# Kernel optimization log

Hardware: AMD Instinct MI355X
Metric: run time of the kernel (lower is better)

The kernel has to match this reference:

```python
import jax, jax.numpy as jnp
import numpy as np

B, S, D, H, F = 2, 2048, 1024, 16, 4096
DK = D // H
EPS = 1e-6


def _ln(x, g, b):
    mu = jnp.mean(x, axis=-1, keepdims=True)
    var = jnp.mean(jnp.square(x - mu), axis=-1, keepdims=True)
    return (x - mu) * jax.lax.rsqrt(var + EPS) * g + b


def setup_inputs() -> dict:
    key = jax.random.key(0)
    ks = jax.random.split(key, 8)
    sc = 0.02
    return {
        "x": jax.random.normal(ks[0], (B, S, D), jnp.float32),
        "wq": jax.random.normal(ks[1], (D, D), jnp.float32) * sc,
        "bq": jnp.zeros((D,), jnp.float32),
        "wk": jax.random.normal(ks[2], (D, D), jnp.float32) * sc,
        "bk": jnp.zeros((D,), jnp.float32),
        "wv": jax.random.normal(ks[3], (D, D), jnp.float32) * sc,
        "bv": jnp.zeros((D,), jnp.float32),
        "wo": jax.random.normal(ks[4], (D, D), jnp.float32) * sc,
        "bo": jnp.zeros((D,), jnp.float32),
        "w1": jax.random.normal(ks[5], (D, F), jnp.float32) * sc,
        "b1": jnp.zeros((F,), jnp.float32),
        "w2": jax.random.normal(ks[6], (F, D), jnp.float32) * sc,
        "b2": jnp.zeros((D,), jnp.float32),
        "g1": jnp.ones((D,), jnp.float32),
        "be1": jnp.zeros((D,), jnp.float32),
        "g2": jnp.ones((D,), jnp.float32),
        "be2": jnp.zeros((D,), jnp.float32),
    }


def reference(x, wq, bq, wk, bk, wv, bv, wo, bo, w1, b1, w2, b2, g1, be1, g2, be2):
    # Multi-head self-attention (no masks, eval-mode dropout = identity)
    q = (x @ wq + bq).reshape(B, S, H, DK)
    k = (x @ wk + bk).reshape(B, S, H, DK)
    v = (x @ wv + bv).reshape(B, S, H, DK)
    scale = 1.0 / (DK ** 0.5)
    score = jnp.einsum('bihd,bjhd->bhij', q, k) * scale  # [B,H,S,S]
    p = jax.nn.softmax(score, axis=-1)
    attn = jnp.einsum('bhij,bjhd->bihd', p, v).reshape(B, S, D)
    attn = attn @ wo + bo
    # residual + LayerNorm 1
    h = _ln(x + attn, g1, be1)
    # FFN (relu) + residual + LayerNorm 2
    ff = jax.nn.relu(h @ w1 + b1) @ w2 + b2
    return _ln(h + ff, g2, be2)
```

## Files before the change

kernel.cpp:

```cpp
#include <hip/hip_runtime.h>
#include <hip/hip_bf16.h>
#include <cmath>

typedef __bf16 bf16_t;
typedef __bf16 bf16x4 __attribute__((ext_vector_type(4)));
typedef __bf16 bf16x8 __attribute__((ext_vector_type(8)));
typedef float  f32x4  __attribute__((ext_vector_type(4)));

__device__ __forceinline__ void gld_lds16(const bf16_t* g, bf16_t* l) {
    __builtin_amdgcn_global_load_lds(
        (const __attribute__((address_space(1))) void*)g,
        (__attribute__((address_space(3))) void*)l,
        16, 0, 0);
}

struct PrepArgs {
    const float* w[6]; bf16_t* wt[6];
    int K[6], N[6], start[6];
    const float* x; bf16_t* xb; int castStart;
    const float* bq; const float* bk; float* bqkv; int biasStart;
};

__global__ __launch_bounds__(256) void prep(PrepArgs pa) {
    __shared__ float tile[32][33];
    const int bid = blockIdx.x, t = threadIdx.x;
    if (bid < pa.castStart) {
        int mi = 0;
#pragma unroll
        for (int i = 1; i < 6; i++) if (bid >= pa.start[i]) mi = i;
        const int tt  = bid - pa.start[mi];
        const int nbx = pa.N[mi] >> 5;
        const int n0 = (tt % nbx) * 32, k0 = (tt / nbx) * 32;
        const float* in = pa.w[mi];
        bf16_t* out = pa.wt[mi];
        const int K = pa.K[mi], N = pa.N[mi];
        const int tx = t & 31, ty = t >> 5;
#pragma unroll
        for (int i = 0; i < 4; i++) {
            int kk = ty + i * 8;
            tile[kk][tx] = in[(size_t)(k0 + kk) * N + n0 + tx];
        }
        __syncthreads();
#pragma unroll
        for (int i = 0; i < 4; i++) {
            int nn = ty + i * 8;
            out[(size_t)(n0 + nn) * K + k0 + tx] = (bf16_t)tile[tx][nn];
        }
    } else if (bid < pa.biasStart) {
        int i = (bid - pa.castStart) * 256 + t;
        f32x4 v = ((const f32x4*)pa.x)[i];
        bf16x4 o;
        o[0] = (bf16_t)v[0]; o[1] = (bf16_t)v[1]; o[2] = (bf16_t)v[2]; o[3] = (bf16_t)v[3];
        ((bf16x4*)pa.xb)[i] = o;
    } else {
#pragma unroll
        for (int j = 0; j < 8; j++) {
            int idx = t * 8 + j;
            pa.bqkv[idx] = idx < 1024 ? pa.bq[idx] : pa.bk[idx - 1024];
        }
    }
}

template<int BN>
__global__ __launch_bounds__(512, 2) void gemm_bt256(
    const bf16_t* __restrict__ A, const bf16_t* __restrict__ Bt,
    const float* __restrict__ bias,
    float* __restrict__ Cf, bf16_t* __restrict__ Cb,
    int M, int N, int lda, int Kloc, int relu, int nbn,
    long bt_bstride, long c_bstride) {
    constexpr int NT = BN / 64;
    constexpr int WN = BN / 4;
    __shared__ __attribute__((aligned(16))) bf16_t As[2][2][256 * 32];
    __shared__ __attribute__((aligned(16))) bf16_t Bs[2][2][BN * 32];
    const int tid  = threadIdx.x;
    const int lane = tid & 63;
    const int wave = tid >> 6;
    const int wm = wave >> 2, wn = wave & 3;
    const int kh = blockIdx.z;

    const int span  = 8 * nbn;
    const int group = blockIdx.x / span;
    const int rem   = blockIdx.x % span;
    const int bm    = group * 8 + (rem & 7);
    const int bn    = rem >> 3;

    const bf16_t* Bt_b = Bt + (size_t)blockIdx.y * bt_bstride;
    float*  Cf_b = Cf ? Cf + (size_t)blockIdx.y * c_bstride + (size_t)kh * M * N : nullptr;
    bf16_t* Cb_b = Cb ? Cb + (size_t)blockIdx.y * c_bstride : nullptr;
    const int koff = kh * Kloc;

    const int r4 = tid >> 2;
    const int kc = (tid & 3) * 8;
    const bf16_t* Ag = A    + (size_t)(bm * 256 + r4) * lda + koff + kc;
    const bf16_t* Bg = Bt_b + (size_t)(bn * BN  + r4) * lda + koff + kc;

    f32x4 acc[8][NT] = {};
    const int mrow = lane & 15;
    const int q8   = (lane >> 4) * 8;

    auto stage = [&](int kk, int buf) {
#pragma unroll
        for (int hh = 0; hh < 2; hh++) {
#pragma unroll
            for (int i = 0; i < 2; i++)
                gld_lds16(Ag + (size_t)(i * 128) * lda + kk + hh * 32,
                          &As[buf][hh][i * 128 * 32] + tid * 8);
            if (BN == 256) {
#pragma unroll
                for (int i = 0; i < 2; i++)
                    gld_lds16(Bg + (size_t)(i * 128) * lda + kk + hh * 32,
                              &Bs[buf][hh][i * 128 * 32] + tid * 8);
            } else {
                gld_lds16(Bg + kk + hh * 32, &Bs[buf][hh][0] + tid * 8);
            }
        }
    };

    stage(0, 0);
    __syncthreads();

    const int nsteps = Kloc >> 6;
    for (int st = 0; st < nsteps; ++st) {
        const int cur = st & 1;
        if (st + 1 < nsteps) stage((st + 1) << 6, cur ^ 1);

#pragma unroll
        for (int hh = 0; hh < 2; hh++) {
            bf16x8 bfr[NT];
#pragma unroll
            for (int n = 0; n < NT; n++)
                bfr[n] = *(const bf16x8*)(&Bs[cur][hh][(wn * WN + n * 16 + mrow) * 32 + q8]);
#pragma unroll
            for (int mt = 0; mt < 8; mt++) {
                bf16x8 af = *(const bf16x8*)(&As[cur][hh][(wm * 128 + mt * 16 + mrow) * 32 + q8]);
#pragma unroll
                for (int n = 0; n < NT; n++)
                    acc[mt][n] = __builtin_amdgcn_mfma_f32_16x16x32_bf16(
                        af, bfr[n], acc[mt][n], 0, 0, 0);
            }
        }
        __syncthreads();
    }

    const int rq = (lane >> 4) * 4;
#pragma unroll
    for (int mt = 0; mt < 8; mt++) {
        int row0 = bm * 256 + wm * 128 + mt * 16 + rq;
#pragma unroll
        for (int n = 0; n < NT; n++) {
            int col = bn * BN + wn * WN + n * 16 + mrow;
            float bvc = (bias && kh == 0) ? bias[col] : 0.f;
#pragma unroll
            for (int r = 0; r < 4; r++) {
                float v = acc[mt][n][r] + bvc;
                if (relu) v = fmaxf(v, 0.f);
                size_t idx = (size_t)(row0 + r) * N + col;
                if (Cf_b) Cf_b[idx] = v;
                if (Cb_b) Cb_b[idx] = (bf16_t)v;
            }
        }
    }
}

template<int MT>
__global__ __launch_bounds__(256) void gemm_bt(
    const bf16_t* __restrict__ A, const bf16_t* __restrict__ Bt,
    const float* __restrict__ bias,
    float* __restrict__ Cf, bf16_t* __restrict__ Cb,
    int M, int N, int lda, int Kloc, int relu, int nbn, int bias_row,
    long bt_bstride, long c_bstride) {
    constexpr int TM = MT * 32;
    __shared__ __attribute__((aligned(16))) bf16_t As[2][TM * 32];
    __shared__ __attribute__((aligned(16))) bf16_t Bs[2][128 * 32];
    const int tid  = threadIdx.x;
    const int lane = tid & 63;
    const int wave = tid >> 6;
    const int wm = wave & 1, wn = wave >> 1;
    const int kh = blockIdx.z;

    const int span  = 8 * nbn;
    const int group = blockIdx.x / span;
    const int rem   = blockIdx.x % span;
    const int bm    = group * 8 + (rem & 7);
    const int bn    = rem >> 3;

    const bf16_t* Bt_b = Bt + (size_t)blockIdx.y * bt_bstride;
    float*  Cf_b = Cf ? Cf + (size_t)blockIdx.y * c_bstride + (size_t)kh * M * N : nullptr;
    bf16_t* Cb_b = Cb ? Cb + (size_t)blockIdx.y * c_bstride : nullptr;
    const int koff = kh * Kloc;

    const int r4 = tid >> 2;
    const int kc = (tid & 3) * 8;
    const bf16_t* Ag = A    + (size_t)(bm * TM  + r4) * lda + koff + kc;
    const bf16_t* Bg = Bt_b + (size_t)(bn * 128 + r4) * lda + koff + kc;

    f32x4 acc[MT][4] = {};
    const int mrow = lane & 15;
    const int q8   = (lane >> 4) * 8;

    auto stage = [&](int kk, int buf) {
#pragma unroll
        for (int i = 0; i < MT / 2; i++)
            gld_lds16(Ag + (size_t)(i * 64) * lda + kk, &As[buf][i * 64 * 32] + tid * 8);
        gld_lds16(Bg + kk,                        &Bs[buf][0] + tid * 8);
        gld_lds16(Bg + (size_t)64 * lda + kk,     &Bs[buf][64 * 32] + tid * 8);
    };

    stage(0, 0);
    __syncthreads();

    const int nt = Kloc >> 5;
    for (int t7 = 0; t7 < nt; ++t7) {
        const int cur = t7 & 1;
        if (t7 + 1 < nt) stage((t7 + 1) << 5, cur ^ 1);

        bf16x8 af[MT], bfr[4];
#pragma unroll
        for (int mt = 0; mt < MT; mt++)
            af[mt] = *(const bf16x8*)(&As[cur][(wm * (MT * 16) + mt * 16 + mrow) * 32 + q8]);
#pragma unroll
        for (int nt2 = 0; nt2 < 4; nt2++)
            bfr[nt2] = *(const bf16x8*)(&Bs[cur][(wn * 64 + nt2 * 16 + mrow) * 32 + q8]);
#pragma unroll
        for (int mt = 0; mt < MT; mt++)
#pragma unroll
            for (int nt2 = 0; nt2 < 4; nt2++)
                acc[mt][nt2] = __builtin_amdgcn_mfma_f32_16x16x32_bf16(
                    af[mt], bfr[nt2], acc[mt][nt2], 0, 0, 0);

        __syncthreads();
    }

    const int rq = (lane >> 4) * 4;
#pragma unroll
    for (int mt = 0; mt < MT; mt++) {
        int row0 = bm * TM + wm * (MT * 16) + mt * 16 + rq;
#pragma unroll
        for (int nt2 = 0; nt2 < 4; nt2++) {
            int col = bn * 128 + wn * 64 + nt2 * 16 + mrow;
            float bvc = (bias && kh == 0 && !bias_row) ? bias[col] : 0.f;
#pragma unroll
            for (int r = 0; r < 4; r++) {
                float bb = (bias && kh == 0 && bias_row) ? bias[row0 + r] : bvc;
                float v = acc[mt][nt2][r] + bb;
                if (relu) v = fmaxf(v, 0.f);
                size_t idx = (size_t)(row0 + r) * N + col;
                if (Cf_b) Cf_b[idx] = v;
                if (Cb_b) Cb_b[idx] = (bf16_t)v;
            }
        }
    }
}

__global__ __launch_bounds__(256) void flash_attn_mfma(
    const bf16_t* __restrict__ QKb,
    const bf16_t* __restrict__ Vtg,
    bf16_t* __restrict__ Outb) {
    __shared__ __attribute__((aligned(16))) bf16_t Ks[2][4096];
    __shared__ __attribute__((aligned(16))) bf16_t Vs[2][4096];
    __shared__ __attribute__((aligned(16))) bf16_t Ps[4096];
    const int t = threadIdx.x;
    const int lane = t & 63, wave = t >> 6;
    const int g = lane >> 4, cl = lane & 15;
    const int b = blockIdx.z, h = blockIdx.y, q0 = blockIdx.x * 64;
    const int RS = 2048;
    const bf16_t* Qg = QKb + (size_t)(b * 2048 + q0) * RS + h * 64;
    const bf16_t* Kg = QKb + (size_t)(b * 2048) * RS + 1024 + h * 64;
    const bf16_t* Vg = Vtg + ((size_t)b * 1024 + h * 64) * 2048;

    const int sr = t >> 2;
    const int sc = (t & 3) * 8;

    const bf16_t* Qrow = Qg + (size_t)(wave * 16 + cl) * RS;
    bf16x8 qr0 = *(const bf16x8*)(Qrow + g * 8);
    bf16x8 qr1 = *(const bf16x8*)(Qrow + 32 + g * 8);

    gld_lds16(Kg + (size_t)sr * RS + sc,        &Ks[0][0]    + t * 8);
    gld_lds16(Kg + (size_t)sr * RS + 32 + sc,   &Ks[0][2048] + t * 8);
    gld_lds16(Vg + (size_t)sr * 2048 + sc,      &Vs[0][0]    + t * 8);
    gld_lds16(Vg + (size_t)sr * 2048 + 32 + sc, &Vs[0][2048] + t * 8);
    __syncthreads();

    f32x4 Oacc[4] = {};
    f32x4 Lacc = {};
    bf16x8 ones;
#pragma unroll
    for (int j = 0; j < 8; j++) ones[j] = (bf16_t)1.0f;

    const int rowb = wave * 16 + cl;
    const int psw  = (cl & 7) << 4;
    char* PsB = (char*)Ps;
    const float C = 0.125f * 1.4426950408889634f;

    for (int kt_i = 0; kt_i < 32; ++kt_i) {
        const int cur = kt_i & 1;
        if (kt_i + 1 < 32) {
            const int nb  = cur ^ 1;
            const int ktn = (kt_i + 1) * 64;
            gld_lds16(Kg + (size_t)(ktn + sr) * RS + sc,        &Ks[nb][0]    + t * 8);
            gld_lds16(Kg + (size_t)(ktn + sr) * RS + 32 + sc,   &Ks[nb][2048] + t * 8);
            gld_lds16(Vg + (size_t)sr * 2048 + ktn + sc,        &Vs[nb][0]    + t * 8);
            gld_lds16(Vg + (size_t)sr * 2048 + ktn + 32 + sc,   &Vs[nb][2048] + t * 8);
        }

        f32x4 Sacc[4] = {};
        __builtin_amdgcn_s_setprio(1);
#pragma unroll
        for (int ks = 0; ks < 2; ++ks) {
            bf16x8 bq = ks ? qr1 : qr0;
#pragma unroll
            for (int mt = 0; mt < 4; ++mt) {
                bf16x8 ak = *(const bf16x8*)(&Ks[cur][ks * 2048 + (mt * 16 + cl) * 32 + g * 8]);
                Sacc[mt] = __builtin_amdgcn_mfma_f32_16x16x32_bf16(ak, bq, Sacc[mt], 0, 0, 0);
            }
        }
        __builtin_amdgcn_s_setprio(0);

#pragma unroll
        for (int mt = 0; mt < 4; ++mt) {
            bf16x4 p4;
#pragma unroll
            for (int r = 0; r < 4; r++)
                p4[r] = (bf16_t)__builtin_amdgcn_exp2f(Sacc[mt][r] * C);
            *(bf16x4*)(PsB + ((rowb * 128 + mt * 32 + g * 8) ^ psw)) = p4;
        }

        __builtin_amdgcn_s_setprio(1);
#pragma unroll
        for (int ks = 0; ks < 2; ++ks) {
            bf16x8 ap = *(const bf16x8*)(PsB + ((rowb * 128 + ks * 64 + g * 16) ^ psw));
            Lacc = __builtin_amdgcn_mfma_f32_16x16x32_bf16(ap, ones, Lacc, 0, 0, 0);
#pragma unroll
            for (int nt = 0; nt < 4; ++nt) {
                bf16x8 bv = *(const bf16x8*)(&Vs[cur][ks * 2048 + (nt * 16 + cl) * 32 + g * 8]);
                Oacc[nt] = __builtin_amdgcn_mfma_f32_16x16x32_bf16(ap, bv, Oacc[nt], 0, 0, 0);
            }
        }
        __builtin_amdgcn_s_setprio(0);

        __syncthreads();
    }

#pragma unroll
    for (int r = 0; r < 4; r++) {
        float inv = 1.f / Lacc[r];
        int qrow = q0 + wave * 16 + g * 4 + r;
        size_t base = (size_t)(b * 2048 + qrow) * 1024 + h * 64;
#pragma unroll
        for (int nt = 0; nt < 4; nt++)
            Outb[base + nt * 16 + cl] = (bf16_t)(Oacc[nt][r] * inv);
    }
}

__global__ __launch_bounds__(256) void resid_ln3(const float* __restrict__ a,
                                                 const float* __restrict__ p0,
                                                 const float* __restrict__ p1,
                                                 const float* __restrict__ g,
                                                 const float* __restrict__ be,
                                                 float* __restrict__ outf,
                                                 bf16_t* __restrict__ outb) {
    const int row = blockIdx.x, t = threadIdx.x;
    const size_t base = (size_t)row * 1024;
    f32x4 v = ((const f32x4*)(a + base))[t] + ((const f32x4*)(p0 + base))[t];
    if (p1) v += ((const f32x4*)(p1 + base))[t];
    float sum = v[0] + v[1] + v[2] + v[3];
    float sq  = v[0] * v[0] + v[1] * v[1] + v[2] * v[2] + v[3] * v[3];
#pragma unroll
    for (int o = 1; o < 64; o <<= 1) {
        sum += __shfl_xor(sum, o);
        sq  += __shfl_xor(sq, o);
    }
    __shared__ float red[8];
    int wave = t >> 6, lane = t & 63;
    if (lane == 0) { red[wave] = sum; red[4 + wave] = sq; }
    __syncthreads();
    sum = red[0] + red[1] + red[2] + red[3];
    sq  = red[4] + red[5] + red[6] + red[7];
    float mu  = sum * (1.f / 1024.f);
    float var = sq * (1.f / 1024.f) - mu * mu;
    float rs  = rsqrtf(var + 1e-6f);
    f32x4 g4 = ((const f32x4*)g)[t];
    f32x4 b4 = ((const f32x4*)be)[t];
    f32x4 o = (v - mu) * rs * g4 + b4;
    ((f32x4*)(outf + base))[t] = o;
    if (outb) {
        bf16x4 ob;
        ob[0] = (bf16_t)o[0]; ob[1] = (bf16_t)o[1]; ob[2] = (bf16_t)o[2]; ob[3] = (bf16_t)o[3];
        ((bf16x4*)(outb + base))[t] = ob;
    }
}

extern "C" void kernel_launch(void* const* d_in, const int* in_sizes, int n_in,
                              void* d_out, int out_size, void* d_ws, size_t ws_size,
                              hipStream_t stream) {
    (void)in_sizes; (void)n_in; (void)out_size; (void)ws_size;
    const float* x   = (const float*)d_in[0];
    const float* wq  = (const float*)d_in[1];
    const float* bq  = (const float*)d_in[2];
    const float* wk  = (const float*)d_in[3];
    const float* bk  = (const float*)d_in[4];
    const float* wv  = (const float*)d_in[5];
    const float* bv  = (const float*)d_in[6];
    const float* wo  = (const float*)d_in[7];
    const float* bo  = (const float*)d_in[8];
    const float* w1  = (const float*)d_in[9];
    const float* b1  = (const float*)d_in[10];
    const float* w2  = (const float*)d_in[11];
    const float* b2  = (const float*)d_in[12];
    const float* g1  = (const float*)d_in[13];
    const float* be1 = (const float*)d_in[14];
    const float* g2  = (const float*)d_in[15];
    const float* be2 = (const float*)d_in[16];
    float* out = (float*)d_out;

    char* ws = (char*)d_ws;
    const size_t MB = 1ull << 20;
    bf16_t* xb    = (bf16_t*)(ws + 0);
    bf16_t* WtQKV = (bf16_t*)(ws + 8 * MB);
    bf16_t* WtO   = (bf16_t*)(ws + 14 * MB);
    bf16_t* Wt1   = (bf16_t*)(ws + 16 * MB);
    bf16_t* Wt2   = (bf16_t*)(ws + 24 * MB);
    float*  bqkv  = (float*)(ws + 32 * MB);
    bf16_t* QKb   = (bf16_t*)(ws + 33 * MB);
    bf16_t* Vt    = (bf16_t*)(ws + 49 * MB);
    bf16_t* ffb   = (bf16_t*)(ws + 33 * MB);
    float*  oa    = (float*)(ws + 65 * MB);
    float*  f2    = (float*)(ws + 65 * MB);
    float*  hbuf  = (float*)(ws + 97 * MB);
    bf16_t* hb    = (bf16_t*)(ws + 113 * MB);
    bf16_t* ab    = xb;
    const int MN = 4096 * 1024;

    PrepArgs pa;
    pa.w[0] = wq; pa.w[1] = wk; pa.w[2] = wv; pa.w[3] = wo; pa.w[4] = w1; pa.w[5] = w2;
    pa.wt[0] = WtQKV; pa.wt[1] = WtQKV + 1024 * 1024; pa.wt[2] = WtQKV + 2048 * 1024;
    pa.wt[3] = WtO; pa.wt[4] = Wt1; pa.wt[5] = Wt2;
    int Ks[6] = {1024, 1024, 1024, 1024, 1024, 4096};
    int Ns[6] = {1024, 1024, 1024, 1024, 4096, 1024};
    int st[6] = {0, 1024, 2048, 3072, 4096, 8192};
    for (int i = 0; i < 6; i++) { pa.K[i] = Ks[i]; pa.N[i] = Ns[i]; pa.start[i] = st[i]; }
    pa.x = x; pa.xb = xb; pa.castStart = 12288;
    pa.bq = bq; pa.bk = bk; pa.bqkv = bqkv; pa.biasStart = 12288 + 4096;
    prep<<<12288 + 4096 + 1, 256, 0, stream>>>(pa);

    gemm_bt256<128><<<256, 512, 0, stream>>>(xb, WtQKV, bqkv, nullptr, QKb,
                                        4096, 2048, 1024, 1024, 0, 16, 0, 0);
    gemm_bt<2><<<dim3(256, 2, 1), 256, 0, stream>>>(WtQKV + 2048 * 1024, xb, bv,
                                        nullptr, Vt, 1024, 2048, 1024, 1024, 0, 16, 1,
                                        (long)2048 * 1024, (long)1024 * 2048);
    flash_attn_mfma<<<dim3(32, 16, 2), 256, 0, stream>>>(QKb, Vt, ab);
    gemm_bt256<128><<<dim3(128, 1, 2), 512, 0, stream>>>(ab, WtO, bo, oa, nullptr,
                                        4096, 1024, 1024, 512, 0, 8, 0, 0);
    resid_ln3<<<4096, 256, 0, stream>>>(x, oa, oa + MN, g1, be1, hbuf, hb);
    gemm_bt256<256><<<256, 512, 0, stream>>>(hb, Wt1, b1, nullptr, ffb,
                                         4096, 4096, 1024, 1024, 1, 16, 0, 0);
    gemm_bt256<128><<<dim3(128, 1, 2), 512, 0, stream>>>(ffb, Wt2, b2, f2, nullptr,
                                        4096, 1024, 4096, 2048, 0, 8, 0, 0);
    resid_ln3<<<4096, 256, 0, stream>>>(hbuf, f2, f2 + MN, g2, be2, out, nullptr);
}
```

Before: 397.9 us.

## Add XOR-swizzled LDS layout to GEMMs and attention, 4-stage pipelined FFN1 GEMM

Applies an XOR swizzle to the 16-byte column slot used when staging tiles into LDS, and matches it on the fragment reads. This targets LDS bank conflicts in all GEMM kernels and in the flash-attention K/V reads. Adds a new gemm_deep kernel for the FFN up-projection with a 4-buffer LDS ring, explicit vmcnt waits so three stages of loads stay in flight, and setprio around the MFMA loop. The deeper ring uses more LDS and forces one block per CU, and the hand-written waitcnt counts must match the number of issued loads exactly.

```diff
diff --git a/kernel.cpp b/kernel.cpp
--- a/kernel.cpp
+++ b/kernel.cpp
@@ -13,6 +13,7 @@
         (__attribute__((address_space(3))) void*)l,
         16, 0, 0);
 }
+
 
 struct PrepArgs {
     const float* w[6]; bf16_t* wt[6];
@@ -57,6 +58,99 @@
         for (int j = 0; j < 8; j++) {
             int idx = t * 8 + j;
             pa.bqkv[idx] = idx < 1024 ? pa.bq[idx] : pa.bk[idx - 1024];
+        }
+    }
+}
+
+__global__ __launch_bounds__(512, 1) void gemm_deep(
+    const bf16_t* __restrict__ A, const bf16_t* __restrict__ Bt,
+    const float* __restrict__ bias, bf16_t* __restrict__ Cb,
+    int N, int lda, int K, int relu, int nbn) {
+    __shared__ __attribute__((aligned(16))) bf16_t As[4][256 * 32];
+    __shared__ __attribute__((aligned(16))) bf16_t Bs[4][256 * 32];
+    const int tid  = threadIdx.x;
+    const int lane = tid & 63;
+    const int wave = tid >> 6;
+    const int wm = wave >> 2, wn = wave & 3;
+
+    const int span  = 8 * nbn;
+    const int group = blockIdx.x / span;
+    const int rem   = blockIdx.x % span;
+    const int bm    = group * 8 + (rem & 7);
+    const int bn    = rem >> 3;
+
+    const int srow   = tid >> 2;
+    const int slot_s = ((tid & 3) ^ ((tid >> 3) & 3)) * 8;
+    const bf16_t* Ag = A  + (size_t)(bm * 256 + srow) * lda + slot_s;
+    const bf16_t* Bg = Bt + (size_t)(bn * 256 + srow) * lda + slot_s;
+
+    auto stage = [&](int kk, int buf) {
+        gld_lds16(Ag + kk,                       &As[buf][0]        + tid * 8);
+        gld_lds16(Ag + (size_t)128 * lda + kk,   &As[buf][128 * 32] + tid * 8);
+        gld_lds16(Bg + kk,                       &Bs[buf][0]        + tid * 8);
+        gld_lds16(Bg + (size_t)128 * lda + kk,   &Bs[buf][128 * 32] + tid * 8);
+    };
+
+    f32x4 acc[8][4] = {};
+    const int mrow = lane & 15;
+    const int qsw  = (((lane >> 4) ^ ((mrow >> 1) & 3))) * 8;
+
+    auto compute = [&](int cur) {
+        bf16x8 bfr[4], af[8];
+#pragma unroll
+        for (int n = 0; n < 4; n++)
+            bfr[n] = *(const bf16x8*)(&Bs[cur][(wn * 64 + n * 16 + mrow) * 32 + qsw]);
+#pragma unroll
+        for (int mt = 0; mt < 8; mt++)
+            af[mt] = *(const bf16x8*)(&As[cur][(wm * 128 + mt * 16 + mrow) * 32 + qsw]);
+        __builtin_amdgcn_s_setprio(1);
+#pragma unroll
+        for (int mt = 0; mt < 8; mt++)
+#pragma unroll
+            for (int n = 0; n < 4; n++)
+                acc[mt][n] = __builtin_amdgcn_mfma_f32_16x16x32_bf16(
+                    af[mt], bfr[n], acc[mt][n], 0, 0, 0);
+        __builtin_amdgcn_s_setprio(0);
+    };
+
+    stage(0, 0); stage(32, 1); stage(64, 2);
+    const int nst = K >> 5;
+    for (int t = 0; t + 3 < nst; ++t) {
+        stage((t + 3) * 32, (t + 3) & 3);
+        asm volatile("s_waitcnt vmcnt(12)" ::: "memory");
+        __builtin_amdgcn_s_barrier();
+        compute(t & 3);
+        asm volatile("s_waitcnt lgkmcnt(0)" ::: "memory");
+        __builtin_amdgcn_s_barrier();
+    }
+    asm volatile("s_waitcnt vmcnt(8)" ::: "memory");
+    __builtin_amdgcn_s_barrier();
+    compute((nst - 3) & 3);
+    asm volatile("s_waitcnt lgkmcnt(0)" ::: "memory");
+    __builtin_amdgcn_s_barrier();
+    asm volatile("s_waitcnt vmcnt(4)" ::: "memory");
+    __builtin_amdgcn_s_barrier();
+    compute((nst - 2) & 3);
+    asm volatile("s_waitcnt lgkmcnt(0)" ::: "memory");
+    __builtin_amdgcn_s_barrier();
+    asm volatile("s_waitcnt vmcnt(0)" ::: "memory");
+    __builtin_amdgcn_s_barrier();
+    compute((nst - 1) & 3);
+
+    const int rq = (lane >> 4) * 4;
+#pragma unroll
+    for (int mt = 0; mt < 8; mt++) {
+        int row0 = bm * 256 + wm * 128 + mt * 16 + rq;
+#pragma unroll
+        for (int n = 0; n < 4; n++) {
+            int col = bn * 256 + wn * 64 + n * 16 + mrow;
+            float bvc = bias ? bias[col] : 0.f;
+#pragma unroll
+            for (int r = 0; r < 4; r++) {
+                float v = acc[mt][n][r] + bvc;
+                if (relu) v = fmaxf(v, 0.f);
+                Cb[(size_t)(row0 + r) * N + col] = (bf16_t)v;
+            }
         }
     }
 }
@@ -90,13 +184,13 @@
     const int koff = kh * Kloc;
 
     const int r4 = tid >> 2;
-    const int kc = (tid & 3) * 8;
-    const bf16_t* Ag = A    + (size_t)(bm * 256 + r4) * lda + koff + kc;
-    const bf16_t* Bg = Bt_b + (size_t)(bn * BN  + r4) * lda + koff + kc;
+    const int kcs = ((tid & 3) ^ ((tid >> 3) & 3)) * 8;
+    const bf16_t* Ag = A    + (size_t)(bm * 256 + r4) * lda + koff + kcs;
+    const bf16_t* Bg = Bt_b + (size_t)(bn * BN  + r4) * lda + koff + kcs;
 
     f32x4 acc[8][NT] = {};
     const int mrow = lane & 15;
-    const int q8   = (lane >> 4) * 8;
+    const int qsw  = (((lane >> 4) ^ ((mrow >> 1) & 3))) * 8;
 
     auto stage = [&](int kk, int buf) {
 #pragma unroll
@@ -129,10 +223,10 @@
             bf16x8 bfr[NT];
 #pragma unroll
             for (int n = 0; n < NT; n++)
-                bfr[n] = *(const bf16x8*)(&Bs[cur][hh][(wn * WN + n * 16 + mrow) * 32 + q8]);
+                bfr[n] = *(const bf16x8*)(&Bs[cur][hh][(wn * WN + n * 16 + mrow) * 32 + qsw]);
 #pragma unroll
             for (int mt = 0; mt < 8; mt++) {
-                bf16x8 af = *(const bf16x8*)(&As[cur][hh][(wm * 128 + mt * 16 + mrow) * 32 + q8]);
+                bf16x8 af = *(const bf16x8*)(&As[cur][hh][(wm * 128 + mt * 16 + mrow) * 32 + qsw]);
 #pragma unroll
                 for (int n = 0; n < NT; n++)
                     acc[mt][n] = __builtin_amdgcn_mfma_f32_16x16x32_bf16(
@@ -190,13 +284,13 @@
     const int koff = kh * Kloc;
 
     const int r4 = tid >> 2;
-    const int kc = (tid & 3) * 8;
-    const bf16_t* Ag = A    + (size_t)(bm * TM  + r4) * lda + koff + kc;
-    const bf16_t* Bg = Bt_b + (size_t)(bn * 128 + r4) * lda + koff + kc;
+    const int kcs = ((tid & 3) ^ ((tid >> 3) & 3)) * 8;
+    const bf16_t* Ag = A    + (size_t)(bm * TM  + r4) * lda + koff + kcs;
+    const bf16_t* Bg = Bt_b + (size_t)(bn * 128 + r4) * lda + koff + kcs;
 
     f32x4 acc[MT][4] = {};
     const int mrow = lane & 15;
-    const int q8   = (lane >> 4) * 8;
+    const int qsw  = (((lane >> 4) ^ ((mrow >> 1) & 3))) * 8;
 
     auto stage = [&](int kk, int buf) {
 #pragma unroll
@@ -217,10 +311,10 @@
         bf16x8 af[MT], bfr[4];
 #pragma unroll
         for (int mt = 0; mt < MT; mt++)
-            af[mt] = *(const bf16x8*)(&As[cur][(wm * (MT * 16) + mt * 16 + mrow) * 32 + q8]);
+            af[mt] = *(const bf16x8*)(&As[cur][(wm * (MT * 16) + mt * 16 + mrow) * 32 + qsw]);
 #pragma unroll
         for (int nt2 = 0; nt2 < 4; nt2++)
-            bfr[nt2] = *(const bf16x8*)(&Bs[cur][(wn * 64 + nt2 * 16 + mrow) * 32 + q8]);
+            bfr[nt2] = *(const bf16x8*)(&Bs[cur][(wn * 64 + nt2 * 16 + mrow) * 32 + qsw]);
 #pragma unroll
         for (int mt = 0; mt < MT; mt++)
 #pragma unroll
@@ -268,17 +362,17 @@
     const bf16_t* Kg = QKb + (size_t)(b * 2048) * RS + 1024 + h * 64;
     const bf16_t* Vg = Vtg + ((size_t)b * 1024 + h * 64) * 2048;
 
-    const int sr = t >> 2;
-    const int sc = (t & 3) * 8;
+    const int sr  = t >> 2;
+    const int scs = (((t & 3) ^ ((t >> 3) & 3))) * 8;
 
     const bf16_t* Qrow = Qg + (size_t)(wave * 16 + cl) * RS;
     bf16x8 qr0 = *(const bf16x8*)(Qrow + g * 8);
     bf16x8 qr1 = *(const bf16x8*)(Qrow + 32 + g * 8);
 
-    gld_lds16(Kg + (size_t)sr * RS + sc,        &Ks[0][0]    + t * 8);
-    gld_lds16(Kg + (size_t)sr * RS + 32 + sc,   &Ks[0][2048] + t * 8);
-    gld_lds16(Vg + (size_t)sr * 2048 + sc,      &Vs[0][0]    + t * 8);
-    gld_lds16(Vg + (size_t)sr * 2048 + 32 + sc, &Vs[0][2048] + t * 8);
+    gld_lds16(Kg + (size_t)sr * RS + scs,        &Ks[0][0]    + t * 8);
+    gld_lds16(Kg + (size_t)sr * RS + 32 + scs,   &Ks[0][2048] + t * 8);
+    gld_lds16(Vg + (size_t)sr * 2048 + scs,      &Vs[0][0]    + t * 8);
+    gld_lds16(Vg + (size_t)sr * 2048 + 32 + scs, &Vs[0][2048] + t * 8);
     __syncthreads();
 
     f32x4 Oacc[4] = {};
@@ -289,6 +383,7 @@
 
     const int rowb = wave * 16 + cl;
     const int psw  = (cl & 7) << 4;
+    const int gsw  = ((g ^ ((cl >> 1) & 3))) * 8;
     char* PsB = (char*)Ps;
     const float C = 0.125f * 1.4426950408889634f;
 
@@ -297,10 +392,10 @@
         if (kt_i + 1 < 32) {
             const int nb  = cur ^ 1;
             const int ktn = (kt_i + 1) * 64;
-            gld_lds16(Kg + (size_t)(ktn + sr) * RS + sc,        &Ks[nb][0]    + t * 8);
-            gld_lds16(Kg + (size_t)(ktn + sr) * RS + 32 + sc,   &Ks[nb][2048] + t * 8);
-            gld_lds16(Vg + (size_t)sr * 2048 + ktn + sc,        &Vs[nb][0]    + t * 8);
-            gld_lds16(Vg + (size_t)sr * 2048 + ktn + 32 + sc,   &Vs[nb][2048] + t * 8);
+            gld_lds16(Kg + (size_t)(ktn + sr) * RS + scs,       &Ks[nb][0]    + t * 8);
+            gld_lds16(Kg + (size_t)(ktn + sr) * RS + 32 + scs,  &Ks[nb][2048] + t * 8);
+            gld_lds16(Vg + (size_t)sr * 2048 + ktn + scs,       &Vs[nb][0]    + t * 8);
+            gld_lds16(Vg + (size_t)sr * 2048 + ktn + 32 + scs,  &Vs[nb][2048] + t * 8);
         }
 
         f32x4 Sacc[4] = {};
@@ -310,7 +405,7 @@
             bf16x8 bq = ks ? qr1 : qr0;
 #pragma unroll
             for (int mt = 0; mt < 4; ++mt) {
-                bf16x8 ak = *(const bf16x8*)(&Ks[cur][ks * 2048 + (mt * 16 + cl) * 32 + g * 8]);
+                bf16x8 ak = *(const bf16x8*)(&Ks[cur][ks * 2048 + (mt * 16 + cl) * 32 + gsw]);
                 Sacc[mt] = __builtin_amdgcn_mfma_f32_16x16x32_bf16(ak, bq, Sacc[mt], 0, 0, 0);
             }
         }
@@ -332,7 +427,7 @@
             Lacc = __builtin_amdgcn_mfma_f32_16x16x32_bf16(ap, ones, Lacc, 0, 0, 0);
 #pragma unroll
             for (int nt = 0; nt < 4; ++nt) {
-                bf16x8 bv = *(const bf16x8*)(&Vs[cur][ks * 2048 + (nt * 16 + cl) * 32 + g * 8]);
+                bf16x8 bv = *(const bf16x8*)(&Vs[cur][ks * 2048 + (nt * 16 + cl) * 32 + gsw]);
                 Oacc[nt] = __builtin_amdgcn_mfma_f32_16x16x32_bf16(ap, bv, Oacc[nt], 0, 0, 0);
             }
         }
@@ -452,8 +547,7 @@
     gemm_bt256<128><<<dim3(128, 1, 2), 512, 0, stream>>>(ab, WtO, bo, oa, nullptr,
                                         4096, 1024, 1024, 512, 0, 8, 0, 0);
     resid_ln3<<<4096, 256, 0, stream>>>(x, oa, oa + MN, g1, be1, hbuf, hb);
-    gemm_bt256<256><<<256, 512, 0, stream>>>(hb, Wt1, b1, nullptr, ffb,
-                                         4096, 4096, 1024, 1024, 1, 16, 0, 0);
+    gemm_deep<<<256, 512, 0, stream>>>(hb, Wt1, b1, ffb, 4096, 1024, 1024, 1, 16);
     gemm_bt256<128><<<dim3(128, 1, 2), 512, 0, stream>>>(ffb, Wt2, b2, f2, nullptr,
                                         4096, 1024, 4096, 2048, 0, 8, 0, 0);
     resid_ln3<<<4096, 256, 0, stream>>>(hbuf, f2, f2 + MN, g2, be2, out, nullptr);
```

Result: no change. 390.2 us (-1.9%).
